# Optimization experiments

Measured on AMD Instinct MI355X. Metric: run time of the kernel, lower is better.

Reference implementation:

```python
import jax, jax.numpy as jnp
import numpy as np

NUM_CAPS_OUT = 10
NUM_NODES = 32 * 6 * 6  # 1152
IN_DIM = 8
OUT_DIM = 16
ROUTING_ITERS = 3


def squash(x):
    # scale = |x|^2/(1+|x|^2); out = scale * x/|x|  (no epsilon, faithful to torch)
    sn = jnp.sum(x * x, axis=-1, keepdims=True)
    return sn / (1.0 + sn) * x / jnp.sqrt(sn)


def setup_inputs() -> dict:
    key = jax.random.key(0)
    ks = jax.random.split(key, 6)
    B = 512
    images = jax.random.normal(ks[0], (B, 1, 28, 28), dtype=jnp.float32)
    # ConvLayer: Conv2d(1, 256, k=9, s=1) with bias
    conv1_w = jax.random.normal(ks[1], (256, 1, 9, 9), dtype=jnp.float32) * 0.05
    conv1_b = jnp.zeros((256,), dtype=jnp.float32)
    prim_w = jax.random.normal(ks[2], (8 * 32, 256, 9, 9), dtype=jnp.float32) * 0.01
    prim_b = jnp.zeros((8 * 32,), dtype=jnp.float32)
    # DigitCaps weight: torch.randn(10, 1152, 8, 16)
    W = jax.random.normal(ks[3], (NUM_CAPS_OUT, NUM_NODES, IN_DIM, OUT_DIM), dtype=jnp.float32)
    return {"images": images, "conv1_w": conv1_w, "conv1_b": conv1_b,
            "prim_w": prim_w, "prim_b": prim_b, "W": W}


def reference(images, conv1_w, conv1_b, prim_w, prim_b, W):
    B = images.shape[0]
    dn = ('NCHW', 'OIHW', 'NCHW')
    # ConvLayer: 28x28 -> 20x20, 256 channels, ReLU
    x = jax.lax.conv_general_dilated(images, conv1_w, (1, 1), 'VALID', dimension_numbers=dn)
    x = jax.nn.relu(x + conv1_b[None, :, None, None])  # [B,256,20,20]
    # PrimaryCaps: 8 stacked convs -> [B, 8*32, 6, 6]; each capsule viewed as (32*6*6,)
    u = jax.lax.conv_general_dilated(x, prim_w, (2, 2), 'VALID', dimension_numbers=dn)
    u = u + prim_b[None, :, None, None]
    u = u.reshape(B, 8, NUM_NODES).transpose(0, 2, 1)  # [B,1152,8]
    u = squash(u)
    # DigitCaps: u_hat[c,b,n,o] = sum_i u[b,n,i] * W[c,n,i,o]
    u_hat = jnp.einsum('bni,cnio->cbno', u, W)  # [10,B,1152,16]
    # Dynamic routing (3 iterations). b_ij kept as [...,1]: torch replicates it
    # across the 16 out dims identically, so math is unchanged.
    b_ij = jnp.zeros(u_hat.shape[:-1] + (1,), dtype=u_hat.dtype)
    v_j = None
    for it in range(ROUTING_ITERS):
        c_ij = jax.nn.softmax(b_ij, axis=2)            # softmax over nodes
        s_j = jnp.sum(c_ij * u_hat, axis=2, keepdims=True)  # [10,B,1,16]
        v_j = squash(s_j)
        if it < ROUTING_ITERS - 1:
            a_ij = jnp.sum(u_hat * v_j, axis=-1, keepdims=True)  # [10,B,1152,1]
            b_ij = b_ij + a_ij
    # squeeze -> [10,B,16], transpose(0,1) -> [B,10,16]
    return v_j[:, :, 0, :].transpose(1, 0, 2)
```

## Files before the change

kernel.cpp:

```cpp
#include <hip/hip_runtime.h>
#include <hip/hip_bf16.h>
#include <cstddef>
#include <cstdint>

typedef __attribute__((ext_vector_type(8))) short v8s;
typedef __attribute__((ext_vector_type(16))) float v16f;

#define GLDS(SRC, DST) __builtin_amdgcn_global_load_lds( \
    (const __attribute__((address_space(1))) void*)(SRC), \
    (__attribute__((address_space(3))) void*)(DST), 16, 0, 0)

__device__ __forceinline__ void bf16split(float x, unsigned short& h, unsigned short& l) {
    union { float f; unsigned u; } a; a.f = x;
    unsigned r = a.u + 0x7fff + ((a.u >> 16) & 1);
    h = (unsigned short)(r >> 16);
    union { unsigned u; float f; } hb; hb.u = (unsigned)h << 16;
    union { float f; unsigned u; } b; b.f = x - hb.f;
    unsigned r2 = b.u + 0x7fff + ((b.u >> 16) & 1);
    l = (unsigned short)(r2 >> 16);
}

__global__ __launch_bounds__(256) void prep_kernel(
    const float* __restrict__ cw, const float* __restrict__ pw,
    float* __restrict__ wT1, char* __restrict__ wpk)
{
    int idx = blockIdx.x * 256 + threadIdx.x;
    if (idx < 81 * 256) {
        int k = idx >> 8, oc = idx & 255;
        wT1[idx] = cw[oc * 81 + k];
    }
    int Q = idx & 2047;
    int slab = idx >> 11;
    int D = Q << 4;
    int R = D >> 9;
    int v = (D & 511) ^ ((R & 31) << 4);
    int h = v >> 7, pl = (v >> 6) & 1, icb = v & 63;
    int ch = h * 64 + R;
    int g = slab / 81, k = slab - g * 81;
    int ic0 = g * 32 + (icb >> 1);
    const float* src = pw + ((size_t)ch * 256 + ic0) * 81 + k;
    v8s ov;
#pragma unroll
    for (int j = 0; j < 8; ++j) {
        unsigned short hh, ll; bf16split(src[(size_t)j * 81], hh, ll);
        ov[j] = (short)(pl ? ll : hh);
    }
    *(v8s*)(wpk + (size_t)slab * 32768 + D) = ov;
}

__global__ __launch_bounds__(256) void conv1_kernel(
    const float* __restrict__ img,
    const float* __restrict__ wT1,
    const float* __restrict__ bias,
    char* __restrict__ xc2,
    int b0)
{
    const int bl = blockIdx.x;
    const int oc = threadIdx.x;
    __shared__ __align__(16) float im[784];
    const float* ib = img + (size_t)(b0 + bl) * 784;
    for (int e = oc; e < 784; e += 256) im[e] = ib[e];
    float w[81];
#pragma unroll
    for (int k = 0; k < 81; ++k) w[k] = wT1[k * 256 + oc];
    float bv = bias[oc];
    __syncthreads();
    char* ob = xc2 + (size_t)bl * 409600;
    for (int oy = 0; oy < 20; ++oy) {
        float a[20];
#pragma unroll
        for (int ox = 0; ox < 20; ++ox) a[ox] = bv;
        for (int ky = 0; ky < 9; ++ky) {
            const float* rp = &im[(oy + ky) * 28];
            float r[28];
#pragma unroll
            for (int q = 0; q < 7; ++q) {
                float4 v4 = *(const float4*)(rp + q * 4);
                r[q * 4] = v4.x; r[q * 4 + 1] = v4.y;
                r[q * 4 + 2] = v4.z; r[q * 4 + 3] = v4.w;
            }
#pragma unroll
            for (int kx = 0; kx < 9; ++kx) {
                float wv = w[ky * 9 + kx];
#pragma unroll
                for (int ox = 0; ox < 20; ++ox)
                    a[ox] = fmaf(wv, r[ox + kx], a[ox]);
            }
        }
#pragma unroll
        for (int ox = 0; ox < 20; ++ox) {
            float av = fmaxf(a[ox], 0.f);
            unsigned short h, l; bf16split(av, h, l);
            char* rp2 = ob + (size_t)(oy * 20 + ox) * 1024;
            *(unsigned short*)(rp2 + oc * 2) = h;
            *(unsigned short*)(rp2 + 512 + oc * 2) = l;
        }
    }
}

__global__ __launch_bounds__(512, 2) void gemm_kernel(
    const char* __restrict__ xc2,
    const char* __restrict__ wpk,
    float* __restrict__ part,
    int M)
{
    __shared__ __align__(128) char As[2][32768];
    __shared__ __align__(128) char Bs[2][32768];
    const int tid = threadIdx.x;
    const int w = tid >> 6, lane = tid & 63;
    const int wm = w & 3, wn = w >> 2;
    const int col = lane & 31, kg = lane >> 5;
    const int id = blockIdx.x;
    const int g = id & 7;
    const int m0 = (id >> 3) * 256;

    int pbase[4], asrc[4];
#pragma unroll
    for (int i = 0; i < 4; ++i) {
        int d = (w * 4 + i) * 1024 + lane * 16;
        int R = d >> 9;
        int v = (d & 511) ^ ((R & 31) << 4);
        int h = v >> 7, pl = (v >> 6) & 1, icb = v & 63;
        int m = m0 + 64 * h + R; if (m >= M) m = M - 1;
        int b = m / 36, s6 = m - b * 36;
        pbase[i] = b * 400 + (s6 / 6) * 40 + (s6 % 6) * 2;
        asrc[i] = pl * 512 + g * 64 + icb;
    }
    const char* wg = wpk + (size_t)g * 81 * 32768;

    v16f acc[2][4];
#pragma unroll
    for (int i = 0; i < 2; ++i)
#pragma unroll
        for (int j = 0; j < 4; ++j)
#pragma unroll
            for (int e = 0; e < 16; ++e) acc[i][j][e] = 0.f;

    auto stage = [&](int nb, int kk) {
        const int koff = (kk / 9) * 20 + (kk % 9);
#pragma unroll
        for (int i = 0; i < 4; ++i)
            GLDS(xc2 + (size_t)(pbase[i] + koff) * 1024 + asrc[i],
                 &As[nb][(w * 4 + i) * 1024]);
        const char* bs = wg + (size_t)kk * 32768;
#pragma unroll
        for (int i = 0; i < 4; ++i)
            GLDS(bs + (w * 4 + i) * 1024 + lane * 16,
                 &Bs[nb][(w * 4 + i) * 1024]);
    };

    stage(0, 0);
    __syncthreads();

    const int xr = col << 4;
    for (int k = 0; k < 81; ++k) {
        const int cur = k & 1;
        if (k < 80) stage(cur ^ 1, k + 1);
        const char* Ab = &As[cur][0];
        const char* Bb = &Bs[cur][0];
#pragma unroll
        for (int s = 0; s < 2; ++s) {
            const int vb = s * 32 + kg * 16;
            v8s Ah[2], Al[2], Bh[4], Bl[4];
#pragma unroll
            for (int fm = 0; fm < 2; ++fm) {
                const char* ap = Ab + (fm * 32 + col) * 512;
                Ah[fm] = *(const v8s*)(ap + ((wm * 128 + vb) ^ xr));
                Al[fm] = *(const v8s*)(ap + ((wm * 128 + 64 + vb) ^ xr));
            }
#pragma unroll
            for (int fn = 0; fn < 4; ++fn) {
                const char* bp = Bb + ((fn & 1) * 32 + col) * 512;
                const int ho = (wn * 2 + (fn >> 1)) * 128;
                Bh[fn] = *(const v8s*)(bp + ((ho + vb) ^ xr));
                Bl[fn] = *(const v8s*)(bp + ((ho + 64 + vb) ^ xr));
            }
            __builtin_amdgcn_s_setprio(1);
#pragma unroll
            for (int fn = 0; fn < 4; ++fn)
#pragma unroll
                for (int fm = 0; fm < 2; ++fm) {
                    acc[fm][fn] = __builtin_amdgcn_mfma_f32_32x32x16_bf16(Al[fm], Bh[fn], acc[fm][fn], 0, 0, 0);
                    acc[fm][fn] = __builtin_amdgcn_mfma_f32_32x32x16_bf16(Ah[fm], Bl[fn], acc[fm][fn], 0, 0, 0);
                    acc[fm][fn] = __builtin_amdgcn_mfma_f32_32x32x16_bf16(Ah[fm], Bh[fn], acc[fm][fn], 0, 0, 0);
                }
            __builtin_amdgcn_s_setprio(0);
        }
        if (k < 80) __syncthreads();
    }

    float* pg = part + (size_t)g * M * 256;
#pragma unroll
    for (int fm = 0; fm < 2; ++fm)
#pragma unroll
        for (int fn = 0; fn < 4; ++fn) {
            int ch = wn * 128 + fn * 32 + col;
#pragma unroll
            for (int rg = 0; rg < 16; ++rg) {
                int row = (rg & 3) + 8 * (rg >> 2) + 4 * kg;
                int m = m0 + wm * 64 + fm * 32 + row;
                if (m < M) pg[(size_t)m * 256 + ch] = acc[fm][fn][rg];
            }
        }
}

__global__ __launch_bounds__(256) void prim2u_kernel(
    const float* __restrict__ part, const float* __restrict__ pb,
    float* __restrict__ u, int M, int b0)
{
    __shared__ float p[64 * 257];
    __shared__ float bsh[256];
    const int tid = threadIdx.x;
    const int rows0 = blockIdx.x * 64;
    bsh[tid] = pb[tid];
#pragma unroll
    for (int j = 0; j < 16; ++j) {
        int e4 = j * 256 + tid;
        int row = e4 >> 6, c4 = (e4 & 63) << 2;
        int rr = rows0 + row; if (rr >= M) rr = M - 1;
        float4 a = make_float4(0.f, 0.f, 0.f, 0.f);
#pragma unroll
        for (int g = 0; g < 8; ++g) {
            float4 v = *(const float4*)(part + ((size_t)g * M + rr) * 256 + c4);
            a.x += v.x; a.y += v.y; a.z += v.z; a.w += v.w;
        }
        float* pp = &p[row * 257 + c4];
        pp[0] = a.x; pp[1] = a.y; pp[2] = a.z; pp[3] = a.w;
    }
    __syncthreads();
#pragma unroll
    for (int j = 0; j < 8; ++j) {
        int idx = j * 256 + tid;
        int row = idx & 63, cc = idx >> 6;
        int m = rows0 + row;
        if (m >= M) continue;
        int b = m / 36, s = m - b * 36;
        float p8[8]; float sn = 0.f;
#pragma unroll
        for (int d = 0; d < 8; ++d) {
            float v = p[row * 257 + d * 32 + cc] + bsh[d * 32 + cc];
            p8[d] = v; sn += v * v;
        }
        float fac = sqrtf(sn) / (1.0f + sn);
        float4 o0, o1;
        o0.x = fac * p8[0]; o0.y = fac * p8[1]; o0.z = fac * p8[2]; o0.w = fac * p8[3];
        o1.x = fac * p8[4]; o1.y = fac * p8[5]; o1.z = fac * p8[6]; o1.w = fac * p8[7];
        float* up = u + ((size_t)(b0 + b) * 1152 + cc * 36 + s) * 8;
        *(float4*)up = o0;
        *(float4*)(up + 4) = o1;
    }
}

__global__ __launch_bounds__(512) void routing_kernel(
    const float* __restrict__ u,
    const float* __restrict__ W,
    float* __restrict__ out,
    int B)
{
    const int b0 = blockIdx.x * 2;
    const int c = blockIdx.y;
    const int tid = threadIdx.x;
    __shared__ float uht[2][16][1152];
    __shared__ float bijs[2][1152];
    __shared__ float red[2][4 * 17];
    __shared__ float sred[2][17];
    __shared__ float mred[2][4];

    const float* __restrict__ Wc = W + (size_t)c * (1152 * 128);
    const int b1 = (b0 + 1 < B) ? b0 + 1 : b0;
    const float* __restrict__ ub0 = u + (size_t)b0 * 9216;
    const float* __restrict__ ub1 = u + (size_t)b1 * 9216;

    for (int n = tid; n < 1152; n += 512) {
        const float4* p0 = (const float4*)(ub0 + n * 8);
        const float4* p1 = (const float4*)(ub1 + n * 8);
        float4 a0 = p0[0], a1 = p0[1], c0 = p1[0], c1 = p1[1];
        float uu0[8] = {a0.x, a0.y, a0.z, a0.w, a1.x, a1.y, a1.z, a1.w};
        float uu1[8] = {c0.x, c0.y, c0.z, c0.w, c1.x, c1.y, c1.z, c1.w};
        float acc0[16], acc1[16];
#pragma unroll
        for (int o = 0; o < 16; ++o) { acc0[o] = 0.f; acc1[o] = 0.f; }
        const float* wn = Wc + n * 128;
#pragma unroll
        for (int i = 0; i < 8; ++i)
#pragma unroll
            for (int o = 0; o < 16; ++o) {
                float wv = wn[i * 16 + o];
                acc0[o] = fmaf(uu0[i], wv, acc0[o]);
                acc1[o] = fmaf(uu1[i], wv, acc1[o]);
            }
#pragma unroll
        for (int o = 0; o < 16; ++o) { uht[0][o][n] = acc0[o]; uht[1][o][n] = acc1[o]; }
        bijs[0][n] = 0.f; bijs[1][n] = 0.f;
    }
    __syncthreads();

    const int img = tid >> 8, t = tid & 255;
    const int wid = t >> 6, lane = t & 63;
    const float* __restrict__ UHT = &uht[img][0][0];
    float* __restrict__ bij = bijs[img];
    float* __restrict__ redi = red[img];
    float* __restrict__ sredi = sred[img];
    float* __restrict__ mredi = mred[img];

    float fac = 0.f, inv = 0.f;
    for (int it = 0; it < 3; ++it) {
        float m = -3.4e38f;
        for (int n = t; n < 1152; n += 256) m = fmaxf(m, bij[n]);
#pragma unroll
        for (int off = 32; off > 0; off >>= 1) m = fmaxf(m, __shfl_down(m, off));
        if (lane == 0) mredi[wid] = m;
        __syncthreads();
        float M = fmaxf(fmaxf(mredi[0], mredi[1]), fmaxf(mredi[2], mredi[3]));
        float se = 0.f;
        float sp[16];
#pragma unroll
        for (int o = 0; o < 16; ++o) sp[o] = 0.f;
        for (int n = t; n < 1152; n += 256) {
            float e = expf(bij[n] - M);
            se += e;
#pragma unroll
            for (int o = 0; o < 16; ++o) sp[o] = fmaf(e, UHT[o * 1152 + n], sp[o]);
        }
#pragma unroll
        for (int o = 0; o < 16; ++o)
#pragma unroll
            for (int off = 32; off > 0; off >>= 1) sp[o] += __shfl_down(sp[o], off);
#pragma unroll
        for (int off = 32; off > 0; off >>= 1) se += __shfl_down(se, off);
        if (lane == 0) {
#pragma unroll
            for (int o = 0; o < 16; ++o) redi[wid * 17 + o] = sp[o];
            redi[wid * 17 + 16] = se;
        }
        __syncthreads();
        if (t < 17)
            sredi[t] = redi[t] + redi[17 + t] + redi[34 + t] + redi[51 + t];
        __syncthreads();
        inv = 1.0f / sredi[16];
        float sn = 0.f;
        float sj[16];
#pragma unroll
        for (int o = 0; o < 16; ++o) { sj[o] = sredi[o] * inv; sn = fmaf(sj[o], sj[o], sn); }
        fac = sqrtf(sn) / (1.0f + sn);
        if (it < 2) {
            float v[16];
#pragma unroll
            for (int o = 0; o < 16; ++o) v[o] = fac * sj[o];
            for (int n = t; n < 1152; n += 256) {
                float a = 0.f;
#pragma unroll
                for (int o = 0; o < 16; ++o) a = fmaf(UHT[o * 1152 + n], v[o], a);
                bij[n] += a;
            }
        }
        __syncthreads();
    }
    if (t < 16 && b0 + img < B)
        out[((size_t)(b0 + img) * 10 + c) * 16 + t] = fac * (sredi[t] * inv);
}

extern "C" void kernel_launch(void* const* d_in, const int* in_sizes, int n_in,
                              void* d_out, int out_size, void* d_ws, size_t ws_size,
                              hipStream_t stream) {
    const float* images  = (const float*)d_in[0];
    const float* conv1_w = (const float*)d_in[1];
    const float* conv1_b = (const float*)d_in[2];
    const float* prim_w  = (const float*)d_in[3];
    const float* prim_b  = (const float*)d_in[4];
    const float* W       = (const float*)d_in[5];
    float* out = (float*)d_out;

    const int B = in_sizes[0] / 784;

    char* wsb = (char*)d_ws;
    float* u = (float*)wsb;
    size_t off = (size_t)B * 1152 * 8 * 4;
    float* wT1 = (float*)(wsb + off);
    off += 81 * 256 * 4;
    off = (off + 1023) & ~(size_t)1023;
    char* wpk = wsb + off;
    off += (size_t)648 * 32768;
    size_t rem = (ws_size > off) ? ws_size - off : 0;
    const size_t perimg = 409600 + 294912;
    int Bc = (int)(rem / perimg);
    if (Bc > B) Bc = B;
    if (Bc >= 32) Bc &= ~31;
    if (Bc < 1) Bc = 1;

    prep_kernel<<<5184, 256, 0, stream>>>(conv1_w, prim_w, wT1, wpk);

    for (int b0 = 0; b0 < B; b0 += Bc) {
        int bc = (B - b0 < Bc) ? (B - b0) : Bc;
        char* xc2 = wsb + off;
        float* part = (float*)(xc2 + (size_t)Bc * 409600);
        conv1_kernel<<<bc, 256, 0, stream>>>(images, wT1, conv1_b, xc2, b0);
        int M = bc * 36;
        int Mtiles = (M + 255) / 256;
        gemm_kernel<<<Mtiles * 8, 512, 0, stream>>>(xc2, wpk, part, M);
        prim2u_kernel<<<(M + 63) / 64, 256, 0, stream>>>(part, prim_b, u, M, b0);
    }
    dim3 rg((B + 1) / 2, 10);
    routing_kernel<<<rg, 512, 0, stream>>>(u, W, out, B);
}
```

Baseline: 1.196 ms.

## Shrink GEMM M-tile to 96 rows with 4 waves for more blocks

Reworks the primary-caps GEMM from a 256x256 tile with 8 waves to a 96x256 tile with 4 waves. Each wave now computes 96 rows by 64 channels, and the A-tile LDS addressing is remapped for 24-row halves. This creates many more blocks, which should fill the CUs better when M is small. It also rebalances the batch chunking so chunks come out even. The cost is lower reuse of B per block, since each block still loads the full 32KB B tile per k-step for only 96 rows, plus more redundant weight traffic.

```diff
diff --git a/kernel.cpp b/kernel.cpp
--- a/kernel.cpp
+++ b/kernel.cpp
@@ -98,55 +98,64 @@
     }
 }
 
-__global__ __launch_bounds__(512, 2) void gemm_kernel(
+__global__ __launch_bounds__(256, 1) void gemm_kernel(
     const char* __restrict__ xc2,
     const char* __restrict__ wpk,
     float* __restrict__ part,
     int M)
 {
-    __shared__ __align__(128) char As[2][32768];
+    __shared__ __align__(128) char As[2][12288];
     __shared__ __align__(128) char Bs[2][32768];
     const int tid = threadIdx.x;
     const int w = tid >> 6, lane = tid & 63;
-    const int wm = w & 3, wn = w >> 2;
+    const int wn = w;
     const int col = lane & 31, kg = lane >> 5;
     const int id = blockIdx.x;
     const int g = id & 7;
-    const int m0 = (id >> 3) * 256;
-
-    int pbase[4], asrc[4];
-#pragma unroll
-    for (int i = 0; i < 4; ++i) {
-        int d = (w * 4 + i) * 1024 + lane * 16;
+    const int m0 = (id >> 3) * 96;
+
+    int pbase[3], asrc[3];
+#pragma unroll
+    for (int i = 0; i < 3; ++i) {
+        int d = (w * 3 + i) * 1024 + lane * 16;
         int R = d >> 9;
         int v = (d & 511) ^ ((R & 31) << 4);
         int h = v >> 7, pl = (v >> 6) & 1, icb = v & 63;
-        int m = m0 + 64 * h + R; if (m >= M) m = M - 1;
+        int m = m0 + 24 * h + R; if (m >= M) m = M - 1;
         int b = m / 36, s6 = m - b * 36;
         pbase[i] = b * 400 + (s6 / 6) * 40 + (s6 % 6) * 2;
         asrc[i] = pl * 512 + g * 64 + icb;
     }
+    int Abase[3], Ahof[3], Axor[3];
+#pragma unroll
+    for (int fm = 0; fm < 3; ++fm) {
+        int m = fm * 32 + col;
+        int h = m / 24, R = m - h * 24;
+        Abase[fm] = R * 512;
+        Ahof[fm] = h * 128;
+        Axor[fm] = R << 4;
+    }
     const char* wg = wpk + (size_t)g * 81 * 32768;
 
-    v16f acc[2][4];
-#pragma unroll
-    for (int i = 0; i < 2; ++i)
-#pragma unroll
-        for (int j = 0; j < 4; ++j)
+    v16f acc[3][2];
+#pragma unroll
+    for (int i = 0; i < 3; ++i)
+#pragma unroll
+        for (int j = 0; j < 2; ++j)
 #pragma unroll
             for (int e = 0; e < 16; ++e) acc[i][j][e] = 0.f;
 
     auto stage = [&](int nb, int kk) {
         const int koff = (kk / 9) * 20 + (kk % 9);
 #pragma unroll
-        for (int i = 0; i < 4; ++i)
+        for (int i = 0; i < 3; ++i)
             GLDS(xc2 + (size_t)(pbase[i] + koff) * 1024 + asrc[i],
-                 &As[nb][(w * 4 + i) * 1024]);
+                 &As[nb][(w * 3 + i) * 1024]);
         const char* bs = wg + (size_t)kk * 32768;
 #pragma unroll
-        for (int i = 0; i < 4; ++i)
-            GLDS(bs + (w * 4 + i) * 1024 + lane * 16,
-                 &Bs[nb][(w * 4 + i) * 1024]);
+        for (int i = 0; i < 8; ++i)
+            GLDS(bs + (w * 8 + i) * 1024 + lane * 16,
+                 &Bs[nb][(w * 8 + i) * 1024]);
     };
 
     stage(0, 0);
@@ -161,25 +170,24 @@
 #pragma unroll
         for (int s = 0; s < 2; ++s) {
             const int vb = s * 32 + kg * 16;
-            v8s Ah[2], Al[2], Bh[4], Bl[4];
-#pragma unroll
-            for (int fm = 0; fm < 2; ++fm) {
-                const char* ap = Ab + (fm * 32 + col) * 512;
-                Ah[fm] = *(const v8s*)(ap + ((wm * 128 + vb) ^ xr));
-                Al[fm] = *(const v8s*)(ap + ((wm * 128 + 64 + vb) ^ xr));
-            }
-#pragma unroll
-            for (int fn = 0; fn < 4; ++fn) {
-                const char* bp = Bb + ((fn & 1) * 32 + col) * 512;
-                const int ho = (wn * 2 + (fn >> 1)) * 128;
-                Bh[fn] = *(const v8s*)(bp + ((ho + vb) ^ xr));
-                Bl[fn] = *(const v8s*)(bp + ((ho + 64 + vb) ^ xr));
+            v8s Ah[3], Al[3], Bh[2], Bl[2];
+#pragma unroll
+            for (int fm = 0; fm < 3; ++fm) {
+                const char* ap = Ab + Abase[fm];
+                Ah[fm] = *(const v8s*)(ap + ((Ahof[fm] + vb) ^ Axor[fm]));
+                Al[fm] = *(const v8s*)(ap + ((Ahof[fm] + 64 + vb) ^ Axor[fm]));
+            }
+#pragma unroll
+            for (int fn = 0; fn < 2; ++fn) {
+                const char* bp = Bb + (fn * 32 + col) * 512;
+                Bh[fn] = *(const v8s*)(bp + ((wn * 128 + vb) ^ xr));
+                Bl[fn] = *(const v8s*)(bp + ((wn * 128 + 64 + vb) ^ xr));
             }
             __builtin_amdgcn_s_setprio(1);
 #pragma unroll
-            for (int fn = 0; fn < 4; ++fn)
-#pragma unroll
-                for (int fm = 0; fm < 2; ++fm) {
+            for (int fn = 0; fn < 2; ++fn)
+#pragma unroll
+                for (int fm = 0; fm < 3; ++fm) {
                     acc[fm][fn] = __builtin_amdgcn_mfma_f32_32x32x16_bf16(Al[fm], Bh[fn], acc[fm][fn], 0, 0, 0);
                     acc[fm][fn] = __builtin_amdgcn_mfma_f32_32x32x16_bf16(Ah[fm], Bl[fn], acc[fm][fn], 0, 0, 0);
                     acc[fm][fn] = __builtin_amdgcn_mfma_f32_32x32x16_bf16(Ah[fm], Bh[fn], acc[fm][fn], 0, 0, 0);
@@ -191,14 +199,14 @@
 
     float* pg = part + (size_t)g * M * 256;
 #pragma unroll
-    for (int fm = 0; fm < 2; ++fm)
-#pragma unroll
-        for (int fn = 0; fn < 4; ++fn) {
-            int ch = wn * 128 + fn * 32 + col;
+    for (int fm = 0; fm < 3; ++fm)
+#pragma unroll
+        for (int fn = 0; fn < 2; ++fn) {
+            int ch = wn * 64 + fn * 32 + col;
 #pragma unroll
             for (int rg = 0; rg < 16; ++rg) {
                 int row = (rg & 3) + 8 * (rg >> 2) + 4 * kg;
-                int m = m0 + wm * 64 + fm * 32 + row;
+                int m = m0 + fm * 32 + row;
                 if (m < M) pg[(size_t)m * 256 + ch] = acc[fm][fn][rg];
             }
         }
@@ -383,10 +391,15 @@
     off += (size_t)648 * 32768;
     size_t rem = (ws_size > off) ? ws_size - off : 0;
     const size_t perimg = 409600 + 294912;
-    int Bc = (int)(rem / perimg);
-    if (Bc > B) Bc = B;
-    if (Bc >= 32) Bc &= ~31;
-    if (Bc < 1) Bc = 1;
+
+    long Bcmax = (long)(rem / perimg);
+    if (Bcmax < 1) Bcmax = 1;
+    if (Bcmax > B) Bcmax = B;
+    int nch = (int)((B + Bcmax - 1) / Bcmax);
+    int Bc = (B + nch - 1) / nch;
+    Bc = (Bc + 31) & ~31;
+    if (Bc > Bcmax) Bc = (int)(Bcmax & ~31L);
+    if (Bc < 1) Bc = (int)Bcmax;
 
     prep_kernel<<<5184, 256, 0, stream>>>(conv1_w, prim_w, wT1, wpk);
 
@@ -396,8 +409,8 @@
         float* part = (float*)(xc2 + (size_t)Bc * 409600);
         conv1_kernel<<<bc, 256, 0, stream>>>(images, wT1, conv1_b, xc2, b0);
         int M = bc * 36;
-        int Mtiles = (M + 255) / 256;
-        gemm_kernel<<<Mtiles * 8, 512, 0, stream>>>(xc2, wpk, part, M);
+        int Mtiles = (M + 95) / 96;
+        gemm_kernel<<<Mtiles * 8, 256, 0, stream>>>(xc2, wpk, part, M);
         prim2u_kernel<<<(M + 63) / 64, 256, 0, stream>>>(part, prim_b, u, M, b0);
     }
     dim3 rg((B + 1) / 2, 10);
```

Result: slower. 1.273 ms (+6.5%).
